# Kernel tuning notes

Hardware: AMD Instinct MI355X
Metric: run time of the kernel (lower is better)

The kernel has to match this reference:

```python
import jax, jax.numpy as jnp
import numpy as np

B, S, H, NH = 2, 2048, 768, 12
HD = H // NH  # 64


def setup_inputs() -> dict:
    key = jax.random.key(0)
    ks = jax.random.split(key, 4)
    scale = 1.0 / np.sqrt(H)
    return {
        "hidden_states": jax.random.normal(ks[0], (B, S, H), dtype=jnp.float32),
        "Wq": jax.random.normal(ks[1], (H, H), dtype=jnp.float32) * scale,
        "bq": jnp.zeros((H,), dtype=jnp.float32),
        "Wk": jax.random.normal(ks[2], (H, H), dtype=jnp.float32) * scale,
        "bk": jnp.zeros((H,), dtype=jnp.float32),
        "Wv": jax.random.normal(ks[3], (H, H), dtype=jnp.float32) * scale,
        "bv": jnp.zeros((H,), dtype=jnp.float32),
    }


def _split_heads(x):
    # [B,S,H] -> [B,NH,S,HD]  (transpose_for_scores)
    b, s, _ = x.shape
    return x.reshape(b, s, NH, HD).transpose(0, 2, 1, 3)


def reference(hidden_states, Wq, bq, Wk, bk, Wv, bv):
    q = _split_heads(hidden_states @ Wq + bq)  # [B,NH,S,HD]
    k = _split_heads(hidden_states @ Wk + bk)
    v = _split_heads(hidden_states @ Wv + bv)
    # delegated attn_fn(q,k,v): scaled-dot-product softmax attention
    scores = jnp.einsum("bhqd,bhkd->bhqk", q, k) / jnp.sqrt(jnp.asarray(HD, q.dtype))
    probs = jax.nn.softmax(scores, axis=-1)
    ctx = jnp.einsum("bhqk,bhkd->bhqd", probs, v)  # [B,NH,S,HD]
    # merge heads back: permute(0,2,1,3) then view to [B,S,H]
    out = ctx.transpose(0, 2, 1, 3).reshape(B, S, NH * HD)
    return out
```

## Files before the change

### kernel.cpp

```cpp
#include <hip/hip_runtime.h>
#include <stdint.h>

typedef __bf16 bf16_t;
typedef __bf16 bf16x8 __attribute__((ext_vector_type(8)));
typedef float f32x4 __attribute__((ext_vector_type(4)));
typedef float f32x16 __attribute__((ext_vector_type(16)));
typedef unsigned int u32x2 __attribute__((ext_vector_type(2)));

#define DEV __device__ __forceinline__

DEV void gload_lds16(const void* g, void* lds) {
  __builtin_amdgcn_global_load_lds(
      (const __attribute__((address_space(1))) uint32_t*)g,
      (__attribute__((address_space(3))) uint32_t*)lds, 16, 0, 0);
}

DEV float fexp2(float x) {
#if __has_builtin(__builtin_amdgcn_exp2f)
  return __builtin_amdgcn_exp2f(x);
#else
  return exp2f(x);
#endif
}

DEV uint32_t pk_bf16(float a, float b) {
  uint32_t lo = (uint32_t)__builtin_bit_cast(uint16_t, (bf16_t)a);
  uint32_t hi = (uint32_t)__builtin_bit_cast(uint16_t, (bf16_t)b);
  return lo | (hi << 16);
}

__global__ __launch_bounds__(256) void cvt_hs(const float* __restrict__ x,
                                              bf16_t* __restrict__ y) {
  int i = blockIdx.x * 256 + threadIdx.x;
  float4 v = ((const float4*)x)[i];
  ((uint2*)y)[i] = make_uint2(pk_bf16(v.x, v.y), pk_bf16(v.z, v.w));
}

__global__ __launch_bounds__(256) void cvt_w(const float* __restrict__ Wq,
                                             const float* __restrict__ Wk,
                                             const float* __restrict__ Wv,
                                             bf16_t* __restrict__ WT) {
  __shared__ float T[32][36];
  const int bx = blockIdx.x;
  const int by = blockIdx.y;
  const int p = bx / 24;
  const float* W = (p == 0) ? Wq : ((p == 1) ? Wk : Wv);
  const int n0 = bx * 32, nn0 = n0 - p * 768, k0 = by * 32;
  const int t = threadIdx.x;
  {
    int r = t >> 3, c4 = (t & 7) * 4;
    float4 v = *(const float4*)&W[(size_t)(k0 + r) * 768 + nn0 + c4];
    T[r][c4 + 0] = v.x; T[r][c4 + 1] = v.y; T[r][c4 + 2] = v.z; T[r][c4 + 3] = v.w;
  }
  __syncthreads();
  {
    int nr = t >> 3, kc = (t & 7) * 4;
    uint32_t lo = pk_bf16(T[kc + 0][nr], T[kc + 1][nr]);
    uint32_t hi = pk_bf16(T[kc + 2][nr], T[kc + 3][nr]);
    *(uint2*)&WT[(size_t)(n0 + nr) * 768 + k0 + kc] = make_uint2(lo, hi);
  }
}

__global__ __launch_bounds__(256) void gemm_qkv(
    const bf16_t* __restrict__ A, const bf16_t* __restrict__ Wt,
    const float* __restrict__ bq, const float* __restrict__ bk,
    const float* __restrict__ bv, bf16_t* __restrict__ Qo,
    bf16_t* __restrict__ Ko, bf16_t* __restrict__ VTo) {
  __shared__ __align__(16) char smem[34816];
  bf16_t* As = (bf16_t*)smem;
  bf16_t* Bs = As + 128 * 64;
  bf16_t* Cs = (bf16_t*)smem;
  const int bx = blockIdx.x;
  const int by = blockIdx.y;
  const int m0 = by * 128, n0 = bx * 128;
  const int tid = threadIdx.x, w = tid >> 6, lane = tid & 63;
  const int mw = (w & 1) * 64, nw = (w >> 1) * 64;
  const int quad = lane >> 4, col = lane & 15;

  f32x4 acc[4][4];
  for (int i = 0; i < 4; i++)
    for (int j = 0; j < 4; j++) acc[i][j] = (f32x4){0.f, 0.f, 0.f, 0.f};

  const int srow = w * 32 + (lane >> 3);
  const int scol = (lane & 7) * 8;
  const bf16_t* ag = A + (size_t)(m0 + srow) * 768 + scol;
  const bf16_t* bg = Wt + (size_t)(n0 + srow) * 768 + scol;

  for (int kk = 0; kk < 12; ++kk) {
    const int k0 = kk * 64;
    __syncthreads();
#pragma unroll
    for (int i = 0; i < 4; i++) {
      gload_lds16(ag + (size_t)i * 8 * 768 + k0, As + (w * 32 + i * 8) * 64);
      gload_lds16(bg + (size_t)i * 8 * 768 + k0, Bs + (w * 32 + i * 8) * 64);
    }
    __syncthreads();
#pragma unroll
    for (int ks = 0; ks < 2; ++ks) {
      bf16x8 af[4], bf[4];
#pragma unroll
      for (int mt = 0; mt < 4; ++mt)
        af[mt] = *(const bf16x8*)&As[(mw + mt * 16 + col) * 64 + ks * 32 + quad * 8];
#pragma unroll
      for (int nt = 0; nt < 4; ++nt)
        bf[nt] = *(const bf16x8*)&Bs[(nw + nt * 16 + col) * 64 + ks * 32 + quad * 8];
#pragma unroll
      for (int mt = 0; mt < 4; ++mt)
#pragma unroll
        for (int nt = 0; nt < 4; ++nt)
          acc[mt][nt] = __builtin_amdgcn_mfma_f32_16x16x32_bf16(
              af[mt], bf[nt], acc[mt][nt], 0, 0, 0);
    }
  }

  const int p = bx / 6;
  const float* bp = (p == 0) ? bq : ((p == 1) ? bk : bv);
  const float kscale = (p == 1) ? 0.18033688011112042f : 1.0f;
  const int bb0 = m0 >> 11, s0 = m0 & 2047;
  __syncthreads();
  if (p < 2) {
#pragma unroll
    for (int nt = 0; nt < 4; nt++) {
      int n = nw + nt * 16 + col;
      float bias = bp[n0 + n - p * 768];
#pragma unroll
      for (int mt = 0; mt < 4; mt++)
#pragma unroll
        for (int r = 0; r < 4; r++) {
          int m = mw + mt * 16 + quad * 4 + r;
          Cs[m * 136 + n] = (bf16_t)((acc[mt][nt][r] + bias) * kscale);
        }
    }
    __syncthreads();
    bf16_t* dst = (p == 0) ? Qo : Ko;
#pragma unroll
    for (int i = 0; i < 8; i++) {
      int idx = i * 256 + tid;
      int m = idx >> 4, c = idx & 15;
      bf16x8 v = *(const bf16x8*)&Cs[m * 136 + c * 8];
      int nn = n0 - p * 768 + c * 8;
      int hq = nn >> 6, hd = nn & 63;
      *(bf16x8*)&dst[(size_t)((bb0 * 12 + hq) * 2048 + s0 + m) * 64 + hd] = v;
    }
  } else {
#pragma unroll
    for (int nt = 0; nt < 4; nt++) {
      int n = nw + nt * 16 + col;
      float bias = bp[n0 + n - 1536];
#pragma unroll
      for (int mt = 0; mt < 4; mt++)
#pragma unroll
        for (int r = 0; r < 4; r++) {
          int m = mw + mt * 16 + quad * 4 + r;
          Cs[n * 136 + m] = (bf16_t)(acc[mt][nt][r] + bias);
        }
    }
    __syncthreads();
#pragma unroll
    for (int i = 0; i < 8; i++) {
      int idx = i * 256 + tid;
      int n = idx >> 4, c = idx & 15;
      bf16x8 v = *(const bf16x8*)&Cs[n * 136 + c * 8];
      int nn = n0 - 1536 + n;
      int hq = nn >> 6, hd = nn & 63;
      *(bf16x8*)&VTo[((size_t)(bb0 * 12 + hq) * 64 + hd) * 2048 + s0 + c * 8] = v;
    }
  }
}

__global__ __launch_bounds__(128) void attn(const bf16_t* __restrict__ Q,
                                            const bf16_t* __restrict__ K,
                                            const bf16_t* __restrict__ VT,
                                            float* __restrict__ out) {
  __shared__ bf16_t Kl[3][64 * 64];
  __shared__ bf16_t Vl[3][64 * 64];
  const int id = blockIdx.x;
  const int r = id >> 3;
  const int bh = (id & 7) * 3 + (r >> 5);
  const int qt = r & 31;
  const int b = bh / 12, head = bh % 12;
  const int tid = threadIdx.x, wv = tid >> 6, lane = tid & 63;
  const int lq = lane & 31, half = lane >> 5;
  const int q0 = qt * 64 + wv * 32;

  bf16x8 qf[4];
#pragma unroll
  for (int ks = 0; ks < 4; ++ks)
    qf[ks] = *(const bf16x8*)&Q[(size_t)(bh * 2048 + q0 + lq) * 64 + ks * 16 + half * 8];

  f32x16 oacc[2];
  for (int i = 0; i < 16; i++) { oacc[0][i] = 0.f; oacc[1][i] = 0.f; }
  float l0 = 0.f, l1 = 0.f, l2 = 0.f, l3 = 0.f;

  const bf16_t* gK = K + (size_t)bh * 2048 * 64;
  const bf16_t* gV = VT + (size_t)bh * 64 * 2048;
  const int srow = lane >> 3, scc = lane & 7;
  const int cg = scc ^ srow;
  const bf16_t* gKb = gK + srow * 64 + cg * 8;
  const bf16_t* gVb = gV + srow * 2048 + cg * 8;

  auto stage = [&](int kb, int buf) {
    if (wv == 0) {
#pragma unroll
      for (int i = 0; i < 8; i++)
        gload_lds16(gKb + kb * 4096 + i * 512, &Kl[buf][i * 512]);
    } else {
#pragma unroll
      for (int i = 0; i < 8; i++)
        gload_lds16(gVb + i * 16384 + kb * 64, &Vl[buf][i * 512]);
    }
  };

  stage(0, 0);
  stage(1, 1);
  asm volatile("s_waitcnt vmcnt(8)" ::: "memory");
  __builtin_amdgcn_s_barrier();
  asm volatile("" ::: "memory");

  int bb = 0, rb = 2;
  for (int kb = 0; kb < 32; ++kb) {
    if (kb < 30) stage(kb + 2, rb);

    f32x16 sacc[2];
    for (int i = 0; i < 16; i++) { sacc[0][i] = 0.f; sacc[1][i] = 0.f; }
    __builtin_amdgcn_s_setprio(1);
#pragma unroll
    for (int t = 0; t < 2; t++) {
      const int row = t * 32 + lq;
#pragma unroll
      for (int ks = 0; ks < 4; ++ks) {
        bf16x8 kf = *(const bf16x8*)&Kl[bb][row * 64 + (((2 * ks + half) ^ (row & 7)) * 8)];
        sacc[t] = __builtin_amdgcn_mfma_f32_32x32x16_bf16(kf, qf[ks], sacc[t], 0, 0, 0);
      }
    }
    __builtin_amdgcn_s_setprio(0);

#pragma unroll
    for (int t = 0; t < 2; t++)
#pragma unroll
      for (int rr = 0; rr < 16; rr++) sacc[t][rr] = fexp2(sacc[t][rr]);
#pragma unroll
    for (int rr = 0; rr < 16; rr += 4) {
      l0 += sacc[0][rr + 0] + sacc[1][rr + 0];
      l1 += sacc[0][rr + 1] + sacc[1][rr + 1];
      l2 += sacc[0][rr + 2] + sacc[1][rr + 2];
      l3 += sacc[0][rr + 3] + sacc[1][rr + 3];
    }

    uint32_t pkq[2][4][2];
#pragma unroll
    for (int t = 0; t < 2; t++)
#pragma unroll
      for (int g = 0; g < 4; g++) {
        pkq[t][g][0] = pk_bf16(sacc[t][4 * g + 0], sacc[t][4 * g + 1]);
        pkq[t][g][1] = pk_bf16(sacc[t][4 * g + 2], sacc[t][4 * g + 3]);
      }

    bf16x8 pfrag[4];
#pragma unroll
    for (int t = 0; t < 2; t++)
#pragma unroll
      for (int e = 0; e < 2; e++) {
        union { uint32_t u[4]; bf16x8 v; } F;
#pragma unroll
        for (int wd = 0; wd < 2; wd++) {
#if __has_builtin(__builtin_amdgcn_permlane32_swap)
          u32x2 sw = __builtin_amdgcn_permlane32_swap(pkq[t][2 * e][wd],
                                                      pkq[t][2 * e + 1][wd],
                                                      false, false);
          F.u[wd] = sw.x;
          F.u[2 + wd] = sw.y;
#else
          uint32_t s = half ? pkq[t][2 * e][wd] : pkq[t][2 * e + 1][wd];
          uint32_t rx = __shfl_xor(s, 32);
          uint32_t ow = half ? pkq[t][2 * e + 1][wd] : pkq[t][2 * e][wd];
          F.u[wd] = half ? rx : ow;
          F.u[2 + wd] = half ? ow : rx;
#endif
        }
        pfrag[2 * t + e] = F.v;
      }

    __builtin_amdgcn_s_setprio(1);
#pragma unroll
    for (int c = 0; c < 4; c++) {
#pragma unroll
      for (int dt = 0; dt < 2; dt++) {
        const int vr = dt * 32 + lq;
        bf16x8 vf = *(const bf16x8*)&Vl[bb][vr * 64 + (((2 * c + half) ^ (vr & 7)) * 8)];
        oacc[dt] = __builtin_amdgcn_mfma_f32_32x32x16_bf16(vf, pfrag[c], oacc[dt], 0, 0, 0);
      }
    }
    __builtin_amdgcn_s_setprio(0);

    if (kb < 30) {
      asm volatile("s_waitcnt vmcnt(8)" ::: "memory");
    } else if (kb == 30) {
      asm volatile("s_waitcnt vmcnt(0)" ::: "memory");
    }
    if (kb < 31) {
      __builtin_amdgcn_s_barrier();
      asm volatile("" ::: "memory");
    }
    bb = (bb == 2) ? 0 : bb + 1;
    rb = (rb == 2) ? 0 : rb + 1;
  }

  float l_own = (l0 + l1) + (l2 + l3);
  float l_tot = l_own + __shfl_xor(l_own, 32);
  float inv = 1.0f / l_tot;
  __syncthreads();
  float* Of = (float*)&Kl[wv][0];
#pragma unroll
  for (int dt = 0; dt < 2; dt++)
#pragma unroll
    for (int rr = 0; rr < 16; rr++) {
      int d = dt * 32 + (rr & 3) + 8 * (rr >> 2) + 4 * half;
      int g = d >> 2, wd = d & 3;
      Of[lq * 64 + ((g ^ (lq & 15)) * 4) + wd] = oacc[dt][rr] * inv;
    }
  float* ob = out + ((size_t)b * 2048 + q0) * 768 + head * 64;
#pragma unroll
  for (int i = 0; i < 8; i++) {
    int idx = i * 64 + lane;
    int q = idx >> 4, c = idx & 15;
    f32x4 v = *(f32x4*)&Of[q * 64 + ((c ^ (q & 15)) * 4)];
    *(f32x4*)&ob[(size_t)q * 768 + c * 4] = v;
  }
}

extern "C" void kernel_launch(void* const* d_in, const int* in_sizes, int n_in,
                              void* d_out, int out_size, void* d_ws, size_t ws_size,
                              hipStream_t stream) {
  const float* hs = (const float*)d_in[0];
  const float* Wq = (const float*)d_in[1];
  const float* bq = (const float*)d_in[2];
  const float* Wk = (const float*)d_in[3];
  const float* bk = (const float*)d_in[4];
  const float* Wv = (const float*)d_in[5];
  const float* bv = (const float*)d_in[6];
  float* out = (float*)d_out;

  char* w = (char*)d_ws;
  bf16_t* hsb = (bf16_t*)w; w += (size_t)4096 * 768 * 2;
  bf16_t* wtb = (bf16_t*)w; w += (size_t)2304 * 768 * 2;
  bf16_t* Qb  = (bf16_t*)w; w += (size_t)24 * 2048 * 64 * 2;
  bf16_t* Kb  = (bf16_t*)w; w += (size_t)24 * 2048 * 64 * 2;
  bf16_t* VTb = (bf16_t*)w;

  hipLaunchKernelGGL(cvt_hs, dim3(3072), dim3(256), 0, stream, hs, hsb);
  hipLaunchKernelGGL(cvt_w, dim3(72, 24), dim3(256), 0, stream, Wq, Wk, Wv, wtb);
  hipLaunchKernelGGL(gemm_qkv, dim3(18, 32), dim3(256), 0, stream, hsb, wtb, bq,
                     bk, bv, Qb, Kb, VTb);
  hipLaunchKernelGGL(attn, dim3(768), dim3(128), 0, stream, Qb, Kb, VTb, out);
}
```

Measured before the change: 173.9 us.

## Split attention KV range across blocks and add combine kernel

Attention blocks now use 4 waves covering 128 queries, and the 2048-key range is split into two halves handled by separate blocks. Each block writes unnormalized fp32 partial outputs and row sums to workspace. A new combine kernel adds the two partials, normalizes, and writes the merged-head output. This shortens the serial key loop per block and raises per-block wave count, at the cost of extra global traffic for partials and an additional kernel launch.

```diff
diff --git a/kernel.cpp b/kernel.cpp
--- a/kernel.cpp
+++ b/kernel.cpp
@@ -168,20 +168,22 @@
   }
 }
 
-__global__ __launch_bounds__(128) void attn(const bf16_t* __restrict__ Q,
-                                            const bf16_t* __restrict__ K,
-                                            const bf16_t* __restrict__ VT,
-                                            float* __restrict__ out) {
-  __shared__ bf16_t Kl[3][64 * 64];
-  __shared__ bf16_t Vl[3][64 * 64];
+__global__ __launch_bounds__(256, 3) void attn(const bf16_t* __restrict__ Q,
+                                               const bf16_t* __restrict__ K,
+                                               const bf16_t* __restrict__ VT,
+                                               float* __restrict__ Op,
+                                               float* __restrict__ lp) {
+  __shared__ __align__(16) char smem[49152];
+  bf16_t* Kl = (bf16_t*)smem;
+  bf16_t* Vl = (bf16_t*)(smem + 24576);
   const int id = blockIdx.x;
-  const int r = id >> 3;
-  const int bh = (id & 7) * 3 + (r >> 5);
-  const int qt = r & 31;
-  const int b = bh / 12, head = bh % 12;
+  const int rr0 = id >> 3;
+  const int bh = (id & 7) * 3 + (rr0 >> 5);
+  const int w5 = rr0 & 31;
+  const int qt = w5 & 15, sp = w5 >> 4;
   const int tid = threadIdx.x, wv = tid >> 6, lane = tid & 63;
   const int lq = lane & 31, half = lane >> 5;
-  const int q0 = qt * 64 + wv * 32;
+  const int q0 = qt * 128 + wv * 32;
 
   bf16x8 qf[4];
 #pragma unroll
@@ -192,34 +194,39 @@
   for (int i = 0; i < 16; i++) { oacc[0][i] = 0.f; oacc[1][i] = 0.f; }
   float l0 = 0.f, l1 = 0.f, l2 = 0.f, l3 = 0.f;
 
-  const bf16_t* gK = K + (size_t)bh * 2048 * 64;
-  const bf16_t* gV = VT + (size_t)bh * 64 * 2048;
+  const bf16_t* gK = K + (size_t)bh * 2048 * 64 + (size_t)sp * 1024 * 64;
+  const bf16_t* gV = VT + (size_t)bh * 64 * 2048 + sp * 1024;
   const int srow = lane >> 3, scc = lane & 7;
   const int cg = scc ^ srow;
   const bf16_t* gKb = gK + srow * 64 + cg * 8;
   const bf16_t* gVb = gV + srow * 2048 + cg * 8;
+  const int kpart = (wv & 1) * 4;
 
   auto stage = [&](int kb, int buf) {
-    if (wv == 0) {
-#pragma unroll
-      for (int i = 0; i < 8; i++)
-        gload_lds16(gKb + kb * 4096 + i * 512, &Kl[buf][i * 512]);
+    if (wv < 2) {
+#pragma unroll
+      for (int i = 0; i < 4; i++) {
+        int ii = kpart + i;
+        gload_lds16(gKb + kb * 4096 + ii * 512, Kl + buf * 4096 + ii * 512);
+      }
     } else {
 #pragma unroll
-      for (int i = 0; i < 8; i++)
-        gload_lds16(gVb + i * 16384 + kb * 64, &Vl[buf][i * 512]);
+      for (int i = 0; i < 4; i++) {
+        int ii = kpart + i;
+        gload_lds16(gVb + (size_t)ii * 16384 + kb * 64, Vl + buf * 4096 + ii * 512);
+      }
     }
   };
 
   stage(0, 0);
   stage(1, 1);
-  asm volatile("s_waitcnt vmcnt(8)" ::: "memory");
+  asm volatile("s_waitcnt vmcnt(4)" ::: "memory");
   __builtin_amdgcn_s_barrier();
   asm volatile("" ::: "memory");
 
   int bb = 0, rb = 2;
-  for (int kb = 0; kb < 32; ++kb) {
-    if (kb < 30) stage(kb + 2, rb);
+  for (int kb = 0; kb < 16; ++kb) {
+    if (kb < 14) stage(kb + 2, rb);
 
     f32x16 sacc[2];
     for (int i = 0; i < 16; i++) { sacc[0][i] = 0.f; sacc[1][i] = 0.f; }
@@ -229,7 +236,7 @@
       const int row = t * 32 + lq;
 #pragma unroll
       for (int ks = 0; ks < 4; ++ks) {
-        bf16x8 kf = *(const bf16x8*)&Kl[bb][row * 64 + (((2 * ks + half) ^ (row & 7)) * 8)];
+        bf16x8 kf = *(const bf16x8*)&Kl[bb * 4096 + row * 64 + (((2 * ks + half) ^ (row & 7)) * 8)];
         sacc[t] = __builtin_amdgcn_mfma_f32_32x32x16_bf16(kf, qf[ks], sacc[t], 0, 0, 0);
       }
     }
@@ -287,18 +294,18 @@
 #pragma unroll
       for (int dt = 0; dt < 2; dt++) {
         const int vr = dt * 32 + lq;
-        bf16x8 vf = *(const bf16x8*)&Vl[bb][vr * 64 + (((2 * c + half) ^ (vr & 7)) * 8)];
+        bf16x8 vf = *(const bf16x8*)&Vl[bb * 4096 + vr * 64 + (((2 * c + half) ^ (vr & 7)) * 8)];
         oacc[dt] = __builtin_amdgcn_mfma_f32_32x32x16_bf16(vf, pfrag[c], oacc[dt], 0, 0, 0);
       }
     }
     __builtin_amdgcn_s_setprio(0);
 
-    if (kb < 30) {
-      asm volatile("s_waitcnt vmcnt(8)" ::: "memory");
-    } else if (kb == 30) {
+    if (kb < 14) {
+      asm volatile("s_waitcnt vmcnt(4)" ::: "memory");
+    } else if (kb == 14) {
       asm volatile("s_waitcnt vmcnt(0)" ::: "memory");
     }
-    if (kb < 31) {
+    if (kb < 15) {
       __builtin_amdgcn_s_barrier();
       asm volatile("" ::: "memory");
     }
@@ -308,25 +315,45 @@
 
   float l_own = (l0 + l1) + (l2 + l3);
   float l_tot = l_own + __shfl_xor(l_own, 32);
-  float inv = 1.0f / l_tot;
   __syncthreads();
-  float* Of = (float*)&Kl[wv][0];
+  float* Of = (float*)smem + wv * 2048;
 #pragma unroll
   for (int dt = 0; dt < 2; dt++)
 #pragma unroll
     for (int rr = 0; rr < 16; rr++) {
       int d = dt * 32 + (rr & 3) + 8 * (rr >> 2) + 4 * half;
       int g = d >> 2, wd = d & 3;
-      Of[lq * 64 + ((g ^ (lq & 15)) * 4) + wd] = oacc[dt][rr] * inv;
-    }
-  float* ob = out + ((size_t)b * 2048 + q0) * 768 + head * 64;
+      Of[lq * 64 + ((g ^ (lq & 15)) * 4) + wd] = oacc[dt][rr];
+    }
+  if (half == 0) lp[((size_t)sp * 24 + bh) * 2048 + q0 + lq] = l_tot;
+  float* ob = Op + (((size_t)sp * 24 + bh) * 2048 + q0) * 64;
 #pragma unroll
   for (int i = 0; i < 8; i++) {
     int idx = i * 64 + lane;
-    int q = idx >> 4, c = idx & 15;
-    f32x4 v = *(f32x4*)&Of[q * 64 + ((c ^ (q & 15)) * 4)];
-    *(f32x4*)&ob[(size_t)q * 768 + c * 4] = v;
-  }
+    int qq = idx >> 4, c = idx & 15;
+    f32x4 v = *(f32x4*)&Of[qq * 64 + ((c ^ (qq & 15)) * 4)];
+    *(f32x4*)&ob[(size_t)qq * 64 + c * 4] = v;
+  }
+}
+
+__global__ __launch_bounds__(256) void combine(const float* __restrict__ Op,
+                                               const float* __restrict__ lp,
+                                               float* __restrict__ out) {
+  int g = blockIdx.x * 256 + threadIdx.x;
+  int bh = g >> 15;
+  int rem = g & 32767;
+  int q = rem >> 4, c = rem & 15;
+  const size_t plane = (size_t)24 * 2048 * 64;
+  size_t o0 = ((size_t)bh * 2048 + q) * 64 + c * 4;
+  f32x4 a = *(const f32x4*)&Op[o0];
+  f32x4 b2 = *(const f32x4*)&Op[plane + o0];
+  float l = lp[bh * 2048 + q] + lp[24 * 2048 + bh * 2048 + q];
+  float inv = 1.0f / l;
+  int b = bh / 12, head = bh % 12;
+  f32x4 r;
+#pragma unroll
+  for (int j = 0; j < 4; j++) r[j] = (a[j] + b2[j]) * inv;
+  *(f32x4*)&out[((size_t)b * 2048 + q) * 768 + head * 64 + c * 4] = r;
 }
 
 extern "C" void kernel_launch(void* const* d_in, const int* in_sizes, int n_in,
@@ -346,11 +373,14 @@
   bf16_t* wtb = (bf16_t*)w; w += (size_t)2304 * 768 * 2;
   bf16_t* Qb  = (bf16_t*)w; w += (size_t)24 * 2048 * 64 * 2;
   bf16_t* Kb  = (bf16_t*)w; w += (size_t)24 * 2048 * 64 * 2;
-  bf16_t* VTb = (bf16_t*)w;
+  bf16_t* VTb = (bf16_t*)w; w += (size_t)24 * 2048 * 64 * 2;
+  float* Opw  = (float*)w;  w += (size_t)2 * 24 * 2048 * 64 * 4;
+  float* lpw  = (float*)w;
 
   hipLaunchKernelGGL(cvt_hs, dim3(3072), dim3(256), 0, stream, hs, hsb);
   hipLaunchKernelGGL(cvt_w, dim3(72, 24), dim3(256), 0, stream, Wq, Wk, Wv, wtb);
   hipLaunchKernelGGL(gemm_qkv, dim3(18, 32), dim3(256), 0, stream, hsb, wtb, bq,
                      bk, bv, Qb, Kb, VTb);
-  hipLaunchKernelGGL(attn, dim3(768), dim3(128), 0, stream, Qb, Kb, VTb, out);
-}
+  hipLaunchKernelGGL(attn, dim3(768), dim3(256), 0, stream, Qb, Kb, VTb, Opw, lpw);
+  hipLaunchKernelGGL(combine, dim3(3072), dim3(256), 0, stream, Opw, lpw, out);
+}
```

Measured after the change: 160.8 us. -7.6%, faster.
